# Kernel optimization log

Hardware: AMD Instinct MI355X
Metric: run time of the kernel (lower is better)

Reference implementation:

```python
import jax, jax.numpy as jnp
import numpy as np

DIM = 1536
NH = 12
HD = DIM // NH  # 128
FF, HH, WW = 32, 8, 12
L = FF * HH * WW  # 3072
WIN = (8, 4, 4)  # block of 128 tokens
BLK = WIN[0] * WIN[1] * WIN[2]


def rms_norm(x, g, eps=1e-5):
    # matches RMSNorm: normalize in fp32, scale by weight
    v = jnp.mean(jnp.square(x), axis=-1, keepdims=True)
    return x * jax.lax.rsqrt(v + eps) * g


def rope(x, freqs, n):
    # x: [B,S,D]; freqs: [S,1,HD/2,2] (cos,sin); complex rotation on pairs
    B, S, D = x.shape
    xr = x.reshape(B, S, n, D // n // 2, 2)
    c, s = freqs[..., 0], freqs[..., 1]        # [S,1,HD/2] broadcast over B,n
    a, b = xr[..., 0], xr[..., 1]
    out = jnp.stack([a * c - b * s, a * s + b * c], axis=-1)
    return out.reshape(B, S, D)


def partition3d(x, f, h, w):
    # [B,f,h,w,D] -> [B, nblocks, 128, D], block order (f/8, h/4, w/4)
    B, D = x.shape[0], x.shape[-1]
    wf, wh, ww = WIN
    x = x.reshape(B, f // wf, wf, h // wh, wh, w // ww, ww, D)
    x = x.transpose(0, 1, 3, 5, 2, 4, 6, 7)
    return x.reshape(B, -1, BLK, D)


def reverse3d(xw, f, h, w):
    # [B, nblocks, 128, D] -> [B, f*h*w, D]
    B, D = xw.shape[0], xw.shape[-1]
    wf, wh, ww = WIN
    x = xw.reshape(B, f // wf, h // wh, w // ww, wf, wh, ww, D)
    x = x.transpose(0, 1, 4, 2, 5, 3, 6, 7)
    return x.reshape(B, f * h * w, D)


def block_mask(f, h, w):
    # build_local_block_mask_3d: spatial mask is all-ones; temporal = context|local
    seqlen = f // WIN[0]
    nb_sp = (h // WIN[1]) * (w // WIN[2])
    stride = WIN[0]
    ctx_idx = (6 + stride - 1) // stride - 1          # context_frames=6
    radius = (5 + stride - 1) // stride               # temp_window_frames=5
    t = jnp.arange(seqlen)
    mt = (t[None, :] <= ctx_idx) | (jnp.abs(t[:, None] - t[None, :]) <= radius)
    # expand temporal block mask over spatial blocks -> [nb, nb]
    return jnp.repeat(jnp.repeat(mt, nb_sp, axis=0), nb_sp, axis=1)


def setup_inputs() -> dict:
    key = jax.random.key(0)
    ks = jax.random.split(key, 8)
    x = jax.random.normal(ks[0], (1, L, DIM), jnp.float32)
    ang = jax.random.uniform(ks[1], (L, 1, HD // 2), jnp.float32, 0.0, 2.0 * np.pi)
    freqs = jnp.stack([jnp.cos(ang), jnp.sin(ang)], axis=-1)  # [L,1,64,2]
    sc = 1.0 / np.sqrt(DIM)
    Wq = jax.random.normal(ks[2], (DIM, DIM), jnp.float32) * sc
    Wk = jax.random.normal(ks[3], (DIM, DIM), jnp.float32) * sc
    Wv = jax.random.normal(ks[4], (DIM, DIM), jnp.float32) * sc
    Wo = jax.random.normal(ks[5], (DIM, DIM), jnp.float32) * sc
    zeros = jnp.zeros((DIM,), jnp.float32)
    ones = jnp.ones((DIM,), jnp.float32)
    return {"x": x, "freqs": freqs, "Wq": Wq, "bq": zeros, "Wk": Wk, "bk": zeros,
            "Wv": Wv, "bv": zeros, "Wo": Wo, "bo": zeros, "g_q": ones, "g_k": ones,
            "f": FF, "h": HH, "w": WW, "local_range": 18}


def reference(x, freqs, Wq, bq, Wk, bk, Wv, bv, Wo, bo, g_q, g_k, f, h, w, local_range):
    B, S, D = x.shape
    q = rms_norm(x @ Wq + bq, g_q, eps=1e-5)
    k = rms_norm(x @ Wk + bk, g_k, eps=1e-5)
    v = x @ Wv + bv
    q = rope(q, freqs, NH)
    k = rope(k, freqs, NH)
    # window partition and flatten back to a reordered sequence
    qs = partition3d(q.reshape(B, f, h, w, D), f, h, w).reshape(B, S, D)
    ks_ = partition3d(k.reshape(B, f, h, w, D), f, h, w).reshape(B, S, D)
    vs = partition3d(v.reshape(B, f, h, w, D), f, h, w).reshape(B, S, D)
    bm = block_mask(f, h, w)                       # [nb, nb] bool
    tok_mask = jnp.repeat(jnp.repeat(bm, BLK, 0), BLK, 1)  # [S, S]
    qh = qs.reshape(B, S, NH, HD).transpose(0, 2, 1, 3)
    kh = ks_.reshape(B, S, NH, HD).transpose(0, 2, 1, 3)
    vh = vs.reshape(B, S, NH, HD).transpose(0, 2, 1, 3)
    scores = jnp.einsum('bhqd,bhkd->bhqk', qh, kh) / np.sqrt(HD)
    scores = jnp.where(tok_mask[None, None], scores, -jnp.inf)
    attn = jax.nn.softmax(scores, axis=-1)
    out = jnp.einsum('bhqk,bhkd->bhqd', attn, vh)
    out = out.transpose(0, 2, 1, 3).reshape(B, S, D)
    out = reverse3d(out.reshape(B, -1, BLK, D), f, h, w)  # undo window reorder
    return out @ Wo + bo
```

## Files before the change

### kernel.cpp

```cpp
#include <hip/hip_runtime.h>
#include <hip/hip_bf16.h>
#include <math.h>

#define S_LEN 3072
#define DMODEL 1536
#define NQKV 4608
#define NHEAD 12
#define HDIM 128
#define NSPLIT 4

typedef __attribute__((ext_vector_type(8))) short bf16x8;
typedef __attribute__((ext_vector_type(4))) float f32x4;
typedef __attribute__((ext_vector_type(4))) unsigned int u32x4;

__device__ __forceinline__ void gload_lds16(const void* g, void* lds) {
  __builtin_amdgcn_global_load_lds(
      (const __attribute__((address_space(1))) unsigned int*)g,
      (__attribute__((address_space(3))) unsigned int*)lds, 16, 0, 0);
}

__device__ __forceinline__ int invperm(int p) {
  int blk = p >> 7;
  int w   = p & 127;
  int fb  = blk / 6;
  int rem = blk - fb * 6;
  int hb  = rem / 3;
  int wb  = rem - hb * 3;
  int fi  = fb * 8 + (w >> 4);
  int hi  = hb * 4 + ((w >> 2) & 3);
  int wi  = wb * 4 + (w & 3);
  return (fi * 8 + hi) * 12 + wi;
}

__device__ __forceinline__ int fwdperm(int s) {
  int fi = s / 96;
  int rem = s - fi * 96;
  int hi = rem / 12;
  int wi = rem - hi * 12;
  int fb = fi >> 3, wf = fi & 7;
  int hb = hi >> 2, wh = hi & 3;
  int wb = wi >> 2, ww = wi & 3;
  return ((fb * 2 + hb) * 3 + wb) * 128 + wf * 16 + wh * 4 + ww;
}

__device__ __forceinline__ void store_out(float* p, float v) { *p = v; }
__device__ __forceinline__ void store_out(__hip_bfloat16* p, float v) { *p = __float2bfloat16(v); }

__global__ __launch_bounds__(256) void convert_bias(
    const float* __restrict__ in, __hip_bfloat16* __restrict__ out,
    const float* __restrict__ bq, const float* __restrict__ bk,
    const float* __restrict__ bv, float* __restrict__ bqkv)
{
  if (blockIdx.x < 4608) {
    int i = blockIdx.x * 256 + threadIdx.x;
    float4 v = ((const float4*)in)[i];
    __hip_bfloat16 b[4] = {__float2bfloat16(v.x), __float2bfloat16(v.y),
                           __float2bfloat16(v.z), __float2bfloat16(v.w)};
    ((ushort4*)out)[i] = *(ushort4*)b;
  } else {
    int j = (blockIdx.x - 4608) * 256 + threadIdx.x;
    float v = (j < 1536) ? bq[j] : (j < 3072) ? bk[j - 1536] : bv[j - 3072];
    bqkv[j] = v;
  }
}

__global__ __launch_bounds__(256) void transpose_convert4(
    const float* __restrict__ W0, const float* __restrict__ W1,
    const float* __restrict__ W2, const float* __restrict__ W3,
    __hip_bfloat16* __restrict__ Wtqkv, __hip_bfloat16* __restrict__ Wot)
{
  __shared__ __hip_bfloat16 Ls[64][67];
  const int z = blockIdx.z;
  const float* W = (z == 0) ? W0 : (z == 1) ? W1 : (z == 2) ? W2 : W3;
  __hip_bfloat16* Wt = (z < 3) ? Wtqkv + (size_t)z * DMODEL * DMODEL : Wot;
  const int r0 = blockIdx.y * 64, c0 = blockIdx.x * 64, t = threadIdx.x;
  {
    int rr = t >> 2, cb = (t & 3) * 16;
    const float4* src = (const float4*)(W + (size_t)(r0 + rr) * DMODEL + c0 + cb);
    #pragma unroll
    for (int i = 0; i < 4; ++i) {
      float4 v = src[i];
      Ls[rr][cb + i * 4 + 0] = __float2bfloat16(v.x);
      Ls[rr][cb + i * 4 + 1] = __float2bfloat16(v.y);
      Ls[rr][cb + i * 4 + 2] = __float2bfloat16(v.z);
      Ls[rr][cb + i * 4 + 3] = __float2bfloat16(v.w);
    }
  }
  __syncthreads();
  {
    int cc = t >> 2, rb = (t & 3) * 16;
    unsigned short tmp[16];
    #pragma unroll
    for (int i = 0; i < 16; ++i) tmp[i] = *(unsigned short*)&Ls[rb + i][cc];
    uint4* dst = (uint4*)(Wt + (size_t)(c0 + cc) * DMODEL + r0 + rb);
    dst[0] = ((uint4*)tmp)[0];
    dst[1] = ((uint4*)tmp)[1];
  }
}

template <typename OutT, int BN>
__global__ __launch_bounds__(256) void gemm_bt(
    const __hip_bfloat16* __restrict__ A, const __hip_bfloat16* __restrict__ Bt,
    const float* __restrict__ bias, OutT* __restrict__ C, int M, int N, int K)
{
  constexpr int NB = BN / 32;
  __shared__ __hip_bfloat16 As[128 * 64];
  __shared__ __hip_bfloat16 Bs[BN * 64];
  const int tid = threadIdx.x, lane = tid & 63, wid = tid >> 6;
  const int l15 = lane & 15, l4 = lane >> 4;
  const int lin = blockIdx.y * gridDim.x + blockIdx.x;
  const int xcd = lin & 7, idx = lin >> 3;
  const int CX = gridDim.x >> 2, CY = gridDim.y >> 1;
  const int cx = xcd & 3, cy = xcd >> 2;
  const int lc = idx % CX, lr = idx / CX;
  const int row0 = (cy * CY + lr) * 128, col0 = (cx * CX + lc) * BN;
  const int wr = (wid >> 1) * 64, wc = (wid & 1) * (BN / 2);

  f32x4 acc[4][NB] = {};
  const char* Ab = (const char*)A;
  const char* Bb = (const char*)Bt;

  auto STAGE = [&](int k0) {
    #pragma unroll
    for (int i = 0; i < 4; ++i) {
      int slot = i * 256 + tid;
      int r = slot >> 3;
      int b = ((slot & 7) * 16) ^ ((r & 7) << 4);
      gload_lds16(Ab + ((size_t)(row0 + r) * K + k0) * 2 + b,
                  (char*)As + slot * 16);
    }
    #pragma unroll
    for (int i = 0; i < BN / 32; ++i) {
      int slot = i * 256 + tid;
      int r = slot >> 3;
      int b = ((slot & 7) * 16) ^ ((r & 7) << 4);
      gload_lds16(Bb + ((size_t)(col0 + r) * K + k0) * 2 + b,
                  (char*)Bs + slot * 16);
    }
  };

  for (int k0 = 0; k0 < K; k0 += 64) {
    STAGE(k0);
    __syncthreads();
    #pragma unroll
    for (int kk = 0; kk < 2; ++kk) {
      bf16x8 a[4], b[NB];
      #pragma unroll
      for (int m = 0; m < 4; ++m) {
        int row = wr + m * 16 + l15;
        int byte = (kk * 64 + l4 * 16) ^ ((row & 7) << 4);
        a[m] = *(const bf16x8*)((const char*)As + row * 128 + byte);
      }
      #pragma unroll
      for (int n = 0; n < NB; ++n) {
        int row = wc + n * 16 + l15;
        int byte = (kk * 64 + l4 * 16) ^ ((row & 7) << 4);
        b[n] = *(const bf16x8*)((const char*)Bs + row * 128 + byte);
      }
      #pragma unroll
      for (int m = 0; m < 4; ++m)
        #pragma unroll
        for (int n = 0; n < NB; ++n)
          acc[m][n] = __builtin_amdgcn_mfma_f32_16x16x32_bf16(a[m], b[n], acc[m][n], 0, 0, 0);
    }
    __syncthreads();
  }

  #pragma unroll
  for (int m = 0; m < 4; ++m) {
    #pragma unroll
    for (int r = 0; r < 4; ++r) {
      size_t row = row0 + wr + m * 16 + l4 * 4 + r;
      #pragma unroll
      for (int n = 0; n < NB; ++n) {
        int col = col0 + wc + n * 16 + l15;
        store_out(&C[row * N + col], acc[m][n][r] + bias[col]);
      }
    }
  }
}

__global__ __launch_bounds__(256) void norm_rope_perm(
    const __hip_bfloat16* __restrict__ X,
    const float* __restrict__ gq, const float* __restrict__ gk,
    const float* __restrict__ freqs,
    __hip_bfloat16* __restrict__ OutQ, __hip_bfloat16* __restrict__ OutK)
{
  const int s = blockIdx.x, tid = threadIdx.x;
  const int sec = blockIdx.y;
  const float* g = sec ? gk : gq;
  __hip_bfloat16* Out = sec ? OutK : OutQ;
  const float qsc = sec ? 1.0f : (0.08838834764831843f * 1.4426950408889634f);
  const unsigned int* row = (const unsigned int*)(X + (size_t)s * NQKV + sec * 1536);
  float e0[3], e1[3];
  float ss = 0.f;
  #pragma unroll
  for (int i = 0; i < 3; ++i) {
    unsigned int u = row[tid + i * 256];
    float a = __uint_as_float(u << 16);
    float b = __uint_as_float(u & 0xffff0000u);
    e0[i] = a; e1[i] = b;
    ss += a * a + b * b;
  }
  #pragma unroll
  for (int off = 32; off > 0; off >>= 1) ss += __shfl_down(ss, off, 64);
  __shared__ float wsum[4];
  if ((tid & 63) == 0) wsum[tid >> 6] = ss;
  __syncthreads();
  float rs = rsqrtf((wsum[0] + wsum[1] + wsum[2] + wsum[3]) * (1.f / DMODEL) + 1e-5f);
  rs *= qsc;
  const int p = fwdperm(s);
  #pragma unroll
  for (int i = 0; i < 3; ++i) {
    int pi = tid + i * 256;
    int n = pi >> 6, d2 = pi & 63;
    float c  = freqs[(size_t)s * 128 + 2 * d2];
    float sn = freqs[(size_t)s * 128 + 2 * d2 + 1];
    float y0 = e0[i] * rs * g[2 * pi];
    float y1 = e1[i] * rs * g[2 * pi + 1];
    float o0 = y0 * c - y1 * sn;
    float o1 = y0 * sn + y1 * c;
    __hip_bfloat16 b0 = __float2bfloat16(o0), b1 = __float2bfloat16(o1);
    unsigned int u = ((unsigned int)(*(unsigned short*)&b1) << 16) | (*(unsigned short*)&b0);
    ((unsigned int*)Out)[(((size_t)n * S_LEN + p) * HDIM + 2 * d2) >> 1] = u;
  }
}

__global__ __launch_bounds__(256) void v_transpose(
    const __hip_bfloat16* __restrict__ Vsec, __hip_bfloat16* __restrict__ Vt)
{
  __shared__ __hip_bfloat16 Ls[64][136];
  const int p0 = blockIdx.x * 64, h = blockIdx.y, t = threadIdx.x;
  {
    int pl = t & 63, dg = t >> 6;
    int sidx = invperm(p0 + pl);
    const uint4* src = (const uint4*)(Vsec + (size_t)sidx * NQKV + h * HDIM + dg * 32);
    #pragma unroll
    for (int i = 0; i < 4; ++i) {
      uint4 v = src[i];
      *(uint4*)&Ls[pl][dg * 32 + i * 8] = v;
    }
  }
  __syncthreads();
  {
    int d = t >> 1, ph = t & 1;
    unsigned short tmp[32];
    #pragma unroll
    for (int i = 0; i < 32; ++i) tmp[i] = *(unsigned short*)&Ls[ph * 32 + i][d];
    uint4* dst = (uint4*)(Vt + ((size_t)h * HDIM + d) * S_LEN + p0 + ph * 32);
    #pragma unroll
    for (int i = 0; i < 4; ++i) dst[i] = ((uint4*)tmp)[i];
  }
}

__global__ __launch_bounds__(512) void attn_mfma(
    const __hip_bfloat16* __restrict__ Qp, const __hip_bfloat16* __restrict__ Kp,
    const __hip_bfloat16* __restrict__ Vt,
    __hip_bfloat16* __restrict__ Opart, float* __restrict__ ml)
{
  __shared__ __hip_bfloat16 Ks[64 * 128];
  __shared__ __hip_bfloat16 Vs[128 * 64];

  const int hw = blockIdx.x;
  const int L  = (hw & 7) * 108 + (hw >> 3);
  const int j  = L % 6;
  const int c  = (L / 6) % 12;
  const int h  = L / 72;
  int tg, split;
  if (c < 2)      { tg = 0; split = c; }
  else if (c < 5) { tg = 1; split = c - 2; }
  else if (c < 9) { tg = 2; split = c - 5; }
  else            { tg = 3; split = c - 9; }
  const int qb = tg * 6 + j;

  const int tid = threadIdx.x, lane = tid & 63, wid = tid >> 6;
  const int l15 = lane & 15, l4 = lane >> 4;

  const int cbegin = split * 12, cend = cbegin + 12;

  const char* Kh = (const char*)(Kp + (size_t)h * S_LEN * HDIM);
  const char* Vh = (const char*)(Vt + (size_t)h * HDIM * S_LEN);

  const int kbase = 8 * (l15 >> 2) + (l15 & 3);
  const int ksw = (((l15 & 3) | (((l15 >> 2) & 1) << 2))) << 4;

  const char* kbp[4];
  #pragma unroll
  for (int dc = 0; dc < 4; ++dc)
    kbp[dc] = (const char*)Ks + kbase * 256 + ((dc * 64 + l4 * 16) ^ ksw);
  const char* vbp[2];
  #pragma unroll
  for (int ks = 0; ks < 2; ++ks)
    vbp[ks] = (const char*)Vs + l15 * 128 + ((ks * 64 + l4 * 16) ^ ((l15 & 7) << 4));

  unsigned int koffA, voffA;
  {
    unsigned int kr = tid >> 4;
    unsigned int sig = (kr & 3) | (((kr >> 3) & 1) << 2);
    koffA = kr * 256 + (((tid & 15) * 16) ^ (sig << 4));
    unsigned int vr = tid >> 3;
    voffA = vr * (S_LEN * 2) + (((tid & 7) * 16) ^ ((vr & 7) << 4));
  }

  auto k0_of = [&](int ci) { return ci * 64 + ((tg == 3 && ci >= 12) ? 768 : 0); };
  auto STAGE = [&](int k0) {
    const char* ks = Kh + (size_t)k0 * 256;
    gload_lds16(ks + koffA,        (char*)Ks + tid * 16);
    gload_lds16(ks + koffA + 8192, (char*)Ks + tid * 16 + 8192);
    const char* vs = Vh + (size_t)k0 * 2 + voffA;
    gload_lds16(vs,                          (char*)Vs + tid * 16);
    gload_lds16(vs + (size_t)64 * S_LEN * 2, (char*)Vs + tid * 16 + 8192);
  };

  bf16x8 aq[4];
  {
    const __hip_bfloat16* qr = Qp + (size_t)h * S_LEN * HDIM
        + (size_t)(qb * 128 + wid * 16 + l15) * HDIM + l4 * 8;
    #pragma unroll
    for (int dc = 0; dc < 4; ++dc) aq[dc] = *(const bf16x8*)(qr + dc * 32);
  }

  f32x4 oacc[8] = {};
  float m2 = -1e30f;
  float lsum = 0.f;

  for (int ci = cbegin; ci < cend; ++ci) {
    const int k0 = k0_of(ci);
    STAGE(k0);
    __syncthreads();

    f32x4 sfr[4] = {};
    __builtin_amdgcn_s_setprio(1);
    #pragma unroll
    for (int ct = 0; ct < 4; ++ct) {
      const int cto = ((ct >> 1) * 32 + (ct & 1) * 4) * 256;
      #pragma unroll
      for (int dc = 0; dc < 4; ++dc) {
        bf16x8 kf = *(const bf16x8*)(kbp[dc] + cto);
        sfr[ct] = __builtin_amdgcn_mfma_f32_16x16x32_bf16(kf, aq[dc], sfr[ct], 0, 0, 0);
      }
    }
    __builtin_amdgcn_s_setprio(0);
    float lmax = fmaxf(
        fmaxf(fmaxf(sfr[0][0], sfr[0][1]), fmaxf(sfr[0][2], sfr[0][3])),
        fmaxf(fmaxf(fmaxf(sfr[1][0], sfr[1][1]), fmaxf(sfr[1][2], sfr[1][3])),
              fmaxf(fmaxf(fmaxf(sfr[2][0], sfr[2][1]), fmaxf(sfr[2][2], sfr[2][3])),
                    fmaxf(fmaxf(sfr[3][0], sfr[3][1]), fmaxf(sfr[3][2], sfr[3][3])))));
    bool grow = lmax > m2 + 8.f;
    if (ci == cbegin || __any(grow)) {
      float mf = lmax;
      mf = fmaxf(mf, __shfl_xor(mf, 16, 64));
      mf = fmaxf(mf, __shfl_xor(mf, 32, 64));
      float mn = fmaxf(m2, mf);
      float corr = exp2f(m2 - mn);
      m2 = mn;
      lsum *= corr;
      float cr[4];
      #pragma unroll
      for (int r = 0; r < 4; ++r) cr[r] = __shfl(corr, l4 * 4 + r, 64);
      #pragma unroll
      for (int n = 0; n < 8; ++n)
        #pragma unroll
        for (int r = 0; r < 4; ++r) oacc[n][r] *= cr[r];
    }
    #pragma unroll
    for (int ct = 0; ct < 4; ++ct)
      #pragma unroll
      for (int r = 0; r < 4; ++r) {
        float p = exp2f(sfr[ct][r] - m2);
        sfr[ct][r] = p;
        lsum += p;
      }
    #pragma unroll
    for (int ks = 0; ks < 2; ++ks) {
      u32x4 wv;
      {
        __hip_bfloat16 a0 = __float2bfloat16(sfr[2 * ks][0]);
        __hip_bfloat16 a1 = __float2bfloat16(sfr[2 * ks][1]);
        __hip_bfloat16 a2 = __float2bfloat16(sfr[2 * ks][2]);
        __hip_bfloat16 a3 = __float2bfloat16(sfr[2 * ks][3]);
        __hip_bfloat16 b0 = __float2bfloat16(sfr[2 * ks + 1][0]);
        __hip_bfloat16 b1 = __float2bfloat16(sfr[2 * ks + 1][1]);
        __hip_bfloat16 b2 = __float2bfloat16(sfr[2 * ks + 1][2]);
        __hip_bfloat16 b3 = __float2bfloat16(sfr[2 * ks + 1][3]);
        wv[0] = ((unsigned int)(*(unsigned short*)&a1) << 16) | (*(unsigned short*)&a0);
        wv[1] = ((unsigned int)(*(unsigned short*)&a3) << 16) | (*(unsigned short*)&a2);
        wv[2] = ((unsigned int)(*(unsigned short*)&b1) << 16) | (*(unsigned short*)&b0);
        wv[3] = ((unsigned int)(*(unsigned short*)&b3) << 16) | (*(unsigned short*)&b2);
      }
      bf16x8 pa = __builtin_bit_cast(bf16x8, wv);
      __builtin_amdgcn_s_setprio(1);
      #pragma unroll
      for (int n = 0; n < 8; ++n) {
        bf16x8 bv = *(const bf16x8*)(vbp[ks] + n * 2048);
        oacc[n] = __builtin_amdgcn_mfma_f32_16x16x32_bf16(pa, bv, oacc[n], 0, 0, 0);
      }
      __builtin_amdgcn_s_setprio(0);
    }
    __syncthreads();
  }

  float t = lsum;
  t += __shfl_xor(t, 16, 64);
  t += __shfl_xor(t, 32, 64);
  float inv = 1.0f / t;
  #pragma unroll
  for (int r = 0; r < 4; ++r) {
    float invr = __shfl(inv, l4 * 4 + r, 64);
    int qrow = qb * 128 + wid * 16 + l4 * 4 + r;
    size_t rowid = (size_t)(split * NHEAD + h) * S_LEN + qrow;
    __hip_bfloat16* dst = Opart + rowid * HDIM;
    #pragma unroll
    for (int n = 0; n < 8; ++n)
      dst[n * 16 + l15] = __float2bfloat16(oacc[n][r] * invr);
  }
  if (lane < 16) {
    int qrow = qb * 128 + wid * 16 + lane;
    size_t rowid = (size_t)(split * NHEAD + h) * S_LEN + qrow;
    ml[rowid * 2 + 0] = m2;
    ml[rowid * 2 + 1] = t;
  }
}

__global__ __launch_bounds__(256) void attn_merge(
    const __hip_bfloat16* __restrict__ Opart, const float* __restrict__ ml,
    __hip_bfloat16* __restrict__ AO)
{
  const int rid = blockIdx.x * 4 + (threadIdx.x >> 6);
  const int lane = threadIdx.x & 63;
  const int h = rid / S_LEN, q = rid - h * S_LEN;
  const int tg = q / 768;
  const int nsp = (tg == 0) ? 2 : (tg == 2) ? 4 : 3;
  size_t rr[NSPLIT];
  float m[NSPLIT], l[NSPLIT];
  float mm = -1e30f;
  #pragma unroll
  for (int s = 0; s < NSPLIT; ++s) {
    rr[s] = (size_t)(s * NHEAD + h) * S_LEN + q;
    bool valid = (s < nsp);
    m[s] = valid ? ml[rr[s] * 2] : -1e30f;
    l[s] = valid ? ml[rr[s] * 2 + 1] : 0.f;
    mm = fmaxf(mm, m[s]);
  }
  float wsum = 0.f, wgt[NSPLIT];
  #pragma unroll
  for (int s = 0; s < NSPLIT; ++s) { wgt[s] = l[s] * exp2f(m[s] - mm); wsum += wgt[s]; }
  float inv = 1.0f / wsum;
  float o0 = 0.f, o1 = 0.f;
  #pragma unroll
  for (int s = 0; s < NSPLIT; ++s) {
    unsigned int u = ((const unsigned int*)(Opart + rr[s] * HDIM))[lane];
    float a = wgt[s] * inv;
    o0 += a * __uint_as_float(u << 16);
    o1 += a * __uint_as_float(u & 0xffff0000u);
  }
  __hip_bfloat16 b0 = __float2bfloat16(o0), b1 = __float2bfloat16(o1);
  unsigned int u = ((unsigned int)(*(unsigned short*)&b1) << 16) | (*(unsigned short*)&b0);
  int sorig = invperm(q);
  ((unsigned int*)(AO + (size_t)sorig * DMODEL + h * HDIM))[lane] = u;
}

extern "C" void kernel_launch(void* const* d_in, const int* in_sizes, int n_in,
                              void* d_out, int out_size, void* d_ws, size_t ws_size,
                              hipStream_t stream)
{
  (void)in_sizes; (void)n_in; (void)out_size; (void)ws_size;
  const float* x     = (const float*)d_in[0];
  const float* freqs = (const float*)d_in[1];
  const float* Wq    = (const float*)d_in[2];
  const float* bq    = (const float*)d_in[3];
  const float* Wk    = (const float*)d_in[4];
  const float* bk    = (const float*)d_in[5];
  const float* Wv    = (const float*)d_in[6];
  const float* bv    = (const float*)d_in[7];
  const float* Wo    = (const float*)d_in[8];
  const float* bo    = (const float*)d_in[9];
  const float* gq    = (const float*)d_in[10];
  const float* gk    = (const float*)d_in[11];
  float* out = (float*)d_out;

  char* w = (char*)d_ws;
  __hip_bfloat16* xbf    = (__hip_bfloat16*)(w);
  __hip_bfloat16* Wtqkv  = (__hip_bfloat16*)(w + 9437184);
  __hip_bfloat16* QKVbf  = (__hip_bfloat16*)(w + 23592960);
  __hip_bfloat16* Qp     = (__hip_bfloat16*)(w + 51904512);
  __hip_bfloat16* Kp     = (__hip_bfloat16*)(w + 61341696);
  __hip_bfloat16* Vtb    = (__hip_bfloat16*)(w + 70778880);
  __hip_bfloat16* AO     = (__hip_bfloat16*)(w + 80216064);
  __hip_bfloat16* Wot    = (__hip_bfloat16*)(w + 89653248);
  float*          bqkv   = (float*)(w + 94371840);
  __hip_bfloat16* Opart  = (__hip_bfloat16*)(w + 9437184);
  float*          mlbuf  = (float*)(w);

  hipLaunchKernelGGL(convert_bias, dim3(4626), dim3(256), 0, stream,
                     x, xbf, bq, bk, bv, bqkv);
  hipLaunchKernelGGL(transpose_convert4, dim3(24, 24, 4), dim3(256), 0, stream,
                     Wq, Wk, Wv, Wo, Wtqkv, Wot);

  hipLaunchKernelGGL((gemm_bt<__hip_bfloat16, 64>), dim3(NQKV / 64, S_LEN / 128),
                     dim3(256), 0, stream, xbf, Wtqkv, bqkv, QKVbf, S_LEN, NQKV, DMODEL);

  hipLaunchKernelGGL(norm_rope_perm, dim3(S_LEN, 2), dim3(256), 0, stream,
                     QKVbf, gq, gk, freqs, Qp, Kp);
  hipLaunchKernelGGL(v_transpose, dim3(48, 12), dim3(256), 0, stream, QKVbf + 3072, Vtb);

  hipLaunchKernelGGL(attn_mfma, dim3(864), dim3(512), 0, stream,
                     Qp, Kp, Vtb, Opart, mlbuf);
  hipLaunchKernelGGL(attn_merge, dim3(S_LEN * NHEAD / 4), dim3(256), 0, stream,
                     Opart, mlbuf, AO);

  hipLaunchKernelGGL((gemm_bt<float, 64>), dim3(DMODEL / 64, S_LEN / 128),
                     dim3(256), 0, stream, AO, Wot, bo, out, S_LEN, DMODEL, DMODEL);
}
```

Baseline: 201.0 us.

## Double-buffer K/V LDS tiles in attention kernel to overlap loads with MFMA

Allocates two LDS buffers each for K and V and prefetches the next chunk while computing on the current one. The per-iteration full wait is replaced with a vmcnt-based partial wait and raw barriers. This hides global-to-LDS latency behind the QK and PV matrix work, at the cost of doubled LDS usage, which may reduce occupancy.

```diff
diff --git a/kernel.cpp b/kernel.cpp
--- a/kernel.cpp
+++ b/kernel.cpp
@@ -258,8 +258,8 @@
     const __hip_bfloat16* __restrict__ Vt,
     __hip_bfloat16* __restrict__ Opart, float* __restrict__ ml)
 {
-  __shared__ __hip_bfloat16 Ks[64 * 128];
-  __shared__ __hip_bfloat16 Vs[128 * 64];
+  __shared__ __hip_bfloat16 Ks[2][64 * 128];
+  __shared__ __hip_bfloat16 Vs[2][64 * 128];
 
   const int hw = blockIdx.x;
   const int L  = (hw & 7) * 108 + (hw >> 3);
@@ -287,11 +287,11 @@
   const char* kbp[4];
   #pragma unroll
   for (int dc = 0; dc < 4; ++dc)
-    kbp[dc] = (const char*)Ks + kbase * 256 + ((dc * 64 + l4 * 16) ^ ksw);
+    kbp[dc] = (const char*)Ks[0] + kbase * 256 + ((dc * 64 + l4 * 16) ^ ksw);
   const char* vbp[2];
   #pragma unroll
   for (int ks = 0; ks < 2; ++ks)
-    vbp[ks] = (const char*)Vs + l15 * 128 + ((ks * 64 + l4 * 16) ^ ((l15 & 7) << 4));
+    vbp[ks] = (const char*)Vs[0] + l15 * 128 + ((ks * 64 + l4 * 16) ^ ((l15 & 7) << 4));
 
   unsigned int koffA, voffA;
   {
@@ -303,13 +303,15 @@
   }
 
   auto k0_of = [&](int ci) { return ci * 64 + ((tg == 3 && ci >= 12) ? 768 : 0); };
-  auto STAGE = [&](int k0) {
+  auto STAGE = [&](int buf, int k0) {
     const char* ks = Kh + (size_t)k0 * 256;
-    gload_lds16(ks + koffA,        (char*)Ks + tid * 16);
-    gload_lds16(ks + koffA + 8192, (char*)Ks + tid * 16 + 8192);
+    char* kd = (char*)Ks[buf];
+    gload_lds16(ks + koffA,        kd + tid * 16);
+    gload_lds16(ks + koffA + 8192, kd + tid * 16 + 8192);
     const char* vs = Vh + (size_t)k0 * 2 + voffA;
-    gload_lds16(vs,                          (char*)Vs + tid * 16);
-    gload_lds16(vs + (size_t)64 * S_LEN * 2, (char*)Vs + tid * 16 + 8192);
+    char* vd = (char*)Vs[buf];
+    gload_lds16(vs,                          vd + tid * 16);
+    gload_lds16(vs + (size_t)64 * S_LEN * 2, vd + tid * 16 + 8192);
   };
 
   bf16x8 aq[4];
@@ -324,10 +326,20 @@
   float m2 = -1e30f;
   float lsum = 0.f;
 
+  STAGE(0, k0_of(cbegin));
+  int cur = 0;
+
   for (int ci = cbegin; ci < cend; ++ci) {
-    const int k0 = k0_of(ci);
-    STAGE(k0);
-    __syncthreads();
+    if (ci + 1 < cend) {
+      STAGE(cur ^ 1, k0_of(ci + 1));
+      asm volatile("s_waitcnt vmcnt(4)" ::: "memory");
+    } else {
+      asm volatile("s_waitcnt vmcnt(0)" ::: "memory");
+    }
+    __builtin_amdgcn_s_barrier();
+    __builtin_amdgcn_sched_barrier(0);
+
+    const int bufoff = cur << 14;
 
     f32x4 sfr[4] = {};
     __builtin_amdgcn_s_setprio(1);
@@ -336,7 +348,7 @@
       const int cto = ((ct >> 1) * 32 + (ct & 1) * 4) * 256;
       #pragma unroll
       for (int dc = 0; dc < 4; ++dc) {
-        bf16x8 kf = *(const bf16x8*)(kbp[dc] + cto);
+        bf16x8 kf = *(const bf16x8*)(kbp[dc] + bufoff + cto);
         sfr[ct] = __builtin_amdgcn_mfma_f32_16x16x32_bf16(kf, aq[dc], sfr[ct], 0, 0, 0);
       }
     }
@@ -392,12 +404,14 @@
       __builtin_amdgcn_s_setprio(1);
       #pragma unroll
       for (int n = 0; n < 8; ++n) {
-        bf16x8 bv = *(const bf16x8*)(vbp[ks] + n * 2048);
+        bf16x8 bv = *(const bf16x8*)(vbp[ks] + bufoff + n * 2048);
         oacc[n] = __builtin_amdgcn_mfma_f32_16x16x32_bf16(pa, bv, oacc[n], 0, 0, 0);
       }
       __builtin_amdgcn_s_setprio(0);
     }
-    __syncthreads();
+    __builtin_amdgcn_sched_barrier(0);
+    __builtin_amdgcn_s_barrier();
+    cur ^= 1;
   }
 
   float t = lsum;
```

After: 199.1 us. Within noise of the previous version (-1.0%).
